# Optimization experiments

Measured on AMD Instinct MI355X. Metric: run time of the kernel, lower is better.

Reference implementation:

```python
import jax, jax.numpy as jnp
import numpy as np

K = 64  # numOnBits

def setup_inputs() -> dict:
    key = jax.random.key(0)
    x = jax.random.normal(key, (8192, 16384), dtype=jnp.float32)
    return {"x": x}

def reference(x) -> jnp.ndarray:
    # Row-wise k-th largest value as threshold, then mask-multiply.
    rows = x.shape[0]
    tmpx = x.reshape(rows, -1)
    topvals, _ = jax.lax.top_k(tmpx, K)        # [rows, K]
    thresh = topvals[:, -1].reshape(rows, *([1] * (x.ndim - 1)))  # k-th largest per row
    comp = (x >= thresh).astype(x.dtype)
    return comp * x
```

## Files before the change

### kernel.cpp

```cpp
#include <hip/hip_runtime.h>

#define ROWLEN 16384
#define NF4 (ROWLEN / 4)
#define KSEL 64u

__device__ __forceinline__ unsigned f2k(float f) {
    unsigned u = __float_as_uint(f);
    return (u & 0x80000000u) ? ~u : (u | 0x80000000u);
}
__device__ __forceinline__ float k2f(unsigned k) {
    unsigned u = (k & 0x80000000u) ? (k ^ 0x80000000u) : ~k;
    return __uint_as_float(u);
}

__global__ __launch_bounds__(256, 4)
void sparsify_topk_kernel(const float* __restrict__ x, float* __restrict__ out, int rows) {
    const int t = threadIdx.x;
    const int row = blockIdx.x;
    if (row >= rows) return;

    __shared__ unsigned hist[256];
    __shared__ unsigned selBin, selK;

    const float4* xrow = (const float4*)(x + (size_t)row * ROWLEN);
    unsigned keys[64];
#pragma unroll
    for (int j = 0; j < 16; ++j) {
        float4 v = xrow[j * 256 + t];
        keys[4 * j + 0] = f2k(v.x);
        keys[4 * j + 1] = f2k(v.y);
        keys[4 * j + 2] = f2k(v.z);
        keys[4 * j + 3] = f2k(v.w);
    }

    unsigned prefix = 0;
    unsigned kcur = KSEL;

#define HPASS(SHIFT, FIRST)                                                    \
    {                                                                          \
        hist[t] = 0;                                                           \
        __syncthreads();                                                       \
        _Pragma("unroll")                                                      \
        for (int e = 0; e < 64; ++e) {                                         \
            unsigned key = keys[e];                                            \
            bool valid = (FIRST) || ((key >> ((SHIFT) + 8)) == prefix);        \
            if (valid) {                                                       \
                unsigned b = (key >> (SHIFT)) & 255u;                          \
                if (hist[b] < KSEL) atomicAdd(&hist[b], 1u);                   \
            }                                                                  \
        }                                                                      \
        __syncthreads();                                                       \
        if (t < 64) {                                                          \
            unsigned c0 = hist[4 * t + 0], c1 = hist[4 * t + 1];               \
            unsigned c2 = hist[4 * t + 2], c3 = hist[4 * t + 3];               \
            unsigned s = c0 + c1 + c2 + c3;                                    \
            _Pragma("unroll")                                                  \
            for (int d = 1; d < 64; d <<= 1) {                                 \
                unsigned v = __shfl_down(s, d);                                \
                if (t + d < 64) s += v;                                        \
            }                                                                  \
            unsigned sAb = __shfl_down(s, 1);                                  \
            if (t == 63) sAb = 0;                                              \
            if (s >= kcur && sAb < kcur) {               \
                unsigned a = sAb;                                              \
                int bin; unsigned kn;                                          \
                if (a + c3 >= kcur)                { bin = 4*t+3; kn = kcur - a; }                    \
                else if (a + c3 + c2 >= kcur)      { bin = 4*t+2; kn = kcur - a - c3; }               \
                else if (a + c3 + c2 + c1 >= kcur) { bin = 4*t+1; kn = kcur - a - c3 - c2; }          \
                else                               { bin = 4*t+0; kn = kcur - a - c3 - c2 - c1; }     \
                selBin = (unsigned)bin;                                        \
                selK = kn;                                                     \
            }                                                                  \
        }                                                                      \
        __syncthreads();                                                       \
        prefix = (prefix << 8) | selBin;                                       \
        kcur = selK;                                                           \
    }

    HPASS(24, true)
    HPASS(16, false)
    HPASS(8, false)
    HPASS(0, false)
#undef HPASS

    const unsigned tkey = prefix;

    float4* orow = (float4*)out + (size_t)row * NF4;
#pragma unroll
    for (int j = 0; j < 16; ++j) {
        unsigned k0 = keys[4 * j + 0], k1 = keys[4 * j + 1];
        unsigned k2 = keys[4 * j + 2], k3 = keys[4 * j + 3];
        float4 o;
        o.x = (k0 >= tkey) ? k2f(k0) : 0.0f;
        o.y = (k1 >= tkey) ? k2f(k1) : 0.0f;
        o.z = (k2 >= tkey) ? k2f(k2) : 0.0f;
        o.w = (k3 >= tkey) ? k2f(k3) : 0.0f;
        orow[j * 256 + t] = o;
    }
}

extern "C" void kernel_launch(void* const* d_in, const int* in_sizes, int n_in,
                              void* d_out, int out_size, void* d_ws, size_t ws_size,
                              hipStream_t stream) {
    const float* x = (const float*)d_in[0];
    float* out = (float*)d_out;
    const int rows = in_sizes[0] / ROWLEN;
    sparsify_topk_kernel<<<rows, 256, 0, stream>>>(x, out, rows);
}
```

Baseline: 848.6 us.

## Replace four radix passes with 12-bit histogram plus candidate rank selection

Swaps the four 8-bit radix-select passes, each with its own histogram, scan and barriers, for a single 12-bit histogram pass laid out as a 4096-entry shared array. The bin holding the k-th key is found with a block-wide scan. Keys falling in that bin are collected into a shared candidate buffer, and the exact threshold is found by brute-force rank counting. The goal is fewer barrier-separated passes over the 64 register-held keys. The cost is an O(n^2) candidate rank step and silent truncation when more than 2048 candidates fall into one bin, which assumes the top-64 boundary bin of this input is small.

```diff
diff --git a/kernel.cpp b/kernel.cpp
--- a/kernel.cpp
+++ b/kernel.cpp
@@ -3,6 +3,7 @@
 #define ROWLEN 16384
 #define NF4 (ROWLEN / 4)
 #define KSEL 64u
+#define CAP  2048u
 
 __device__ __forceinline__ unsigned f2k(float f) {
     unsigned u = __float_as_uint(f);
@@ -14,13 +15,16 @@
 }
 
 __global__ __launch_bounds__(256, 4)
-void sparsify_topk_kernel(const float* __restrict__ x, float* __restrict__ out, int rows) {
+void sparsify_topk_kernel(const float* __restrict__ x, float* __restrict__ out) {
     const int t = threadIdx.x;
     const int row = blockIdx.x;
-    if (row >= rows) return;
+    const int lane = t & 63, w = t >> 6;
 
-    __shared__ unsigned hist[256];
-    __shared__ unsigned selBin, selK;
+    __shared__ unsigned hist[4096];
+    __shared__ unsigned cand[CAP];
+    __shared__ unsigned ncand;
+    __shared__ unsigned wtot[4];
+    __shared__ unsigned selPrefix, selK, tkeySh;
 
     const float4* xrow = (const float4*)(x + (size_t)row * ROWLEN);
     unsigned keys[64];
@@ -33,67 +37,80 @@
         keys[4 * j + 3] = f2k(v.w);
     }
 
-    unsigned prefix = 0;
-    unsigned kcur = KSEL;
+#pragma unroll
+    for (int i = 0; i < 16; ++i) hist[i * 256 + t] = 0;
+    if (t == 0) ncand = 0;
+    __syncthreads();
 
-#define HPASS(SHIFT, FIRST)                                                    \
-    {                                                                          \
-        hist[t] = 0;                                                           \
-        __syncthreads();                                                       \
-        _Pragma("unroll")                                                      \
-        for (int e = 0; e < 64; ++e) {                                         \
-            unsigned key = keys[e];                                            \
-            bool valid = (FIRST) || ((key >> ((SHIFT) + 8)) == prefix);        \
-            if (valid) {                                                       \
-                unsigned b = (key >> (SHIFT)) & 255u;                          \
-                if (hist[b] < KSEL) atomicAdd(&hist[b], 1u);                   \
-            }                                                                  \
-        }                                                                      \
-        __syncthreads();                                                       \
-        if (t < 64) {                                                          \
-            unsigned c0 = hist[4 * t + 0], c1 = hist[4 * t + 1];               \
-            unsigned c2 = hist[4 * t + 2], c3 = hist[4 * t + 3];               \
-            unsigned s = c0 + c1 + c2 + c3;                                    \
-            _Pragma("unroll")                                                  \
-            for (int d = 1; d < 64; d <<= 1) {                                 \
-                unsigned v = __shfl_down(s, d);                                \
-                if (t + d < 64) s += v;                                        \
-            }                                                                  \
-            unsigned sAb = __shfl_down(s, 1);                                  \
-            if (t == 63) sAb = 0;                                              \
-            if (s >= kcur && sAb < kcur) {               \
-                unsigned a = sAb;                                              \
-                int bin; unsigned kn;                                          \
-                if (a + c3 >= kcur)                { bin = 4*t+3; kn = kcur - a; }                    \
-                else if (a + c3 + c2 >= kcur)      { bin = 4*t+2; kn = kcur - a - c3; }               \
-                else if (a + c3 + c2 + c1 >= kcur) { bin = 4*t+1; kn = kcur - a - c3 - c2; }          \
-                else                               { bin = 4*t+0; kn = kcur - a - c3 - c2 - c1; }     \
-                selBin = (unsigned)bin;                                        \
-                selK = kn;                                                     \
-            }                                                                  \
-        }                                                                      \
-        __syncthreads();                                                       \
-        prefix = (prefix << 8) | selBin;                                       \
-        kcur = selK;                                                           \
+#pragma unroll
+    for (int e = 0; e < 64; ++e) {
+        unsigned b = keys[e] >> 20;
+        atomicAdd(&hist[(b & 15u) * 256u + (b >> 4)], 1u);
     }
+    __syncthreads();
 
-    HPASS(24, true)
-    HPASS(16, false)
-    HPASS(8, false)
-    HPASS(0, false)
-#undef HPASS
+    unsigned s = 0;
+#pragma unroll
+    for (int i = 0; i < 16; ++i) s += hist[i * 256 + t];
 
-    const unsigned tkey = prefix;
+    unsigned incl = s;
+#pragma unroll
+    for (int d = 1; d < 64; d <<= 1) {
+        unsigned v = __shfl_down(incl, d);
+        if (lane + d < 64) incl += v;
+    }
+    if (lane == 0) wtot[w] = incl;
+    __syncthreads();
+
+    unsigned above = incl - s;
+    for (int w2 = w + 1; w2 < 4; ++w2) above += wtot[w2];
+
+    if (above < KSEL && above + s >= KSEL) {
+        unsigned A = above;
+#pragma unroll
+        for (int i = 15; i >= 0; --i) {
+            unsigned c = hist[i * 256 + t];
+            if (A + c >= KSEL) { selPrefix = ((unsigned)t << 4) | (unsigned)i;
+                                 selK = KSEL - A; break; }
+            A += c;
+        }
+    }
+    __syncthreads();
+
+    const unsigned pfx = selPrefix;
+    const unsigned k2 = selK;
+#pragma unroll
+    for (int e = 0; e < 64; ++e) {
+        if ((keys[e] >> 20) == pfx) {
+            unsigned idx = atomicAdd(&ncand, 1u);
+            if (idx < CAP) cand[idx] = keys[e];
+        }
+    }
+    __syncthreads();
+
+    unsigned n = ncand; if (n > CAP) n = CAP;
+    for (unsigned i = t; i < n; i += 256) {
+        unsigned ki = cand[i];
+        unsigned gt = 0, ge = 0;
+        for (unsigned j = 0; j < n; ++j) {
+            unsigned kj = cand[j];
+            gt += (kj > ki);
+            ge += (kj >= ki);
+        }
+        if (gt < k2 && ge >= k2) tkeySh = ki;
+    }
+    __syncthreads();
+    const unsigned tkey = tkeySh;
 
     float4* orow = (float4*)out + (size_t)row * NF4;
 #pragma unroll
     for (int j = 0; j < 16; ++j) {
         unsigned k0 = keys[4 * j + 0], k1 = keys[4 * j + 1];
-        unsigned k2 = keys[4 * j + 2], k3 = keys[4 * j + 3];
+        unsigned kk2 = keys[4 * j + 2], k3 = keys[4 * j + 3];
         float4 o;
         o.x = (k0 >= tkey) ? k2f(k0) : 0.0f;
         o.y = (k1 >= tkey) ? k2f(k1) : 0.0f;
-        o.z = (k2 >= tkey) ? k2f(k2) : 0.0f;
+        o.z = (kk2 >= tkey) ? k2f(kk2) : 0.0f;
         o.w = (k3 >= tkey) ? k2f(k3) : 0.0f;
         orow[j * 256 + t] = o;
     }
@@ -105,5 +122,5 @@
     const float* x = (const float*)d_in[0];
     float* out = (float*)d_out;
     const int rows = in_sizes[0] / ROWLEN;
-    sparsify_topk_kernel<<<rows, 256, 0, stream>>>(x, out, rows);
+    sparsify_topk_kernel<<<rows, 256, 0, stream>>>(x, out);
 }
```

Measured after the change: 851.7 us. Within noise of the previous version (+0.4%).
